# Performance work log

Measured on AMD Instinct MI355X. Metric: run time of the kernel, lower is better.

Reference implementation:

```python
import jax, jax.numpy as jnp
import numpy as np

N, D, B, E, H = 512, 32, 4, 256, 4
SEP = 256
HD = E // H


def setup_inputs() -> dict:
    key = jax.random.key(0)
    ks = jax.random.split(key, 8)
    s = 0.02
    return {
        "src": jax.random.normal(ks[0], (N, D, B, E), dtype=jnp.float32),
        "w_in_row": jax.random.normal(ks[1], (3 * E, E), dtype=jnp.float32) * s,
        "b_in_row": jnp.zeros((3 * E,), jnp.float32),
        "w_out_row": jax.random.normal(ks[2], (E, E), dtype=jnp.float32) * s,
        "b_out_row": jnp.zeros((E,), jnp.float32),
        "w_in_col": jax.random.normal(ks[3], (3 * E, E), dtype=jnp.float32) * s,
        "b_in_col": jnp.zeros((3 * E,), jnp.float32),
        "w_out_col": jax.random.normal(ks[4], (E, E), dtype=jnp.float32) * s,
        "b_out_col": jnp.zeros((E,), jnp.float32),
        "ln_g": jnp.ones((E,), jnp.float32),
        "ln_b": jnp.zeros((E,), jnp.float32),
        "task_ids": jax.random.randint(ks[5], (B,), 0, 10),
        "single_eval_position": SEP,
    }


def _mha(x, w_in, b_in, w_out, b_out, mask):
    # x: (S, Bt, E); torch MultiheadAttention with batch_first=False
    S, Bt, _ = x.shape
    qkv = x @ w_in.T + b_in                      # (S, Bt, 3E)
    q, k, v = jnp.split(qkv, 3, axis=-1)
    to_heads = lambda t: t.reshape(S, Bt, H, HD).transpose(1, 2, 0, 3)  # (Bt,H,S,HD)
    q, k, v = to_heads(q), to_heads(k), to_heads(v)
    scores = jnp.einsum('bhqd,bhkd->bhqk', q, k) * (HD ** -0.5)
    if mask is not None:  # mask True == disallowed (torch convention)
        scores = jnp.where(mask[None, None], -jnp.inf, scores)
    attn = jax.nn.softmax(scores, axis=-1)
    out = jnp.einsum('bhqk,bhkd->bhqd', attn, v)
    out = out.transpose(2, 0, 1, 3).reshape(S, Bt, E)
    return out @ w_out.T + b_out


def _layer_norm(x, g, b, eps=1e-5):
    mu = x.mean(-1, keepdims=True)
    var = ((x - mu) ** 2).mean(-1, keepdims=True)
    return (x - mu) / jnp.sqrt(var + eps) * g + b


def reference(src, w_in_row, b_in_row, w_out_row, b_out_row,
              w_in_col, b_in_col, w_out_col, b_out_col,
              ln_g, ln_b, task_ids, single_eval_position):
    sep = single_eval_position
    idx = jnp.arange(N)
    # block mask: test queries may not attend to test keys
    row_mask = (idx[:, None] >= sep) & (idx[None, :] >= sep)
    # row attention over the N axis, batched across D*B
    src_row = _mha(src.reshape(N, D * B, E), w_in_row, b_in_row,
                   w_out_row, b_out_row, row_mask).reshape(N, D, B, E)
    # column attention over the D axis, batched across N*B (no mask)
    x_col = src.transpose(1, 0, 2, 3).reshape(D, N * B, E)
    src_col = _mha(x_col, w_in_col, b_in_col, w_out_col, b_out_col,
                   None).reshape(D, N, B, E).transpose(1, 0, 2, 3)
    # parallel axial (seq_axial=False), post-norm (pre_norm=False): row_norm unused
    return _layer_norm(src + src_row + src_col, ln_g, ln_b)
```

## Files before the change

kernel.cpp:

```cpp
#include <hip/hip_runtime.h>
#include <hip/hip_bf16.h>
#include <cstdint>
#include <cstddef>


typedef __hip_bfloat16 bf16;
typedef __attribute__((ext_vector_type(8))) short bf16x8;
typedef __attribute__((ext_vector_type(8))) short short8;
typedef __attribute__((ext_vector_type(4))) short bf16x4;
typedef __attribute__((ext_vector_type(4))) float f32x4;

#define NN 512
#define DD 32
#define BB 4
#define EE 256
#define HH 4
#define HDIM 64
#define DB (DD*BB)
#define MTOK (NN*DD*BB)
#define KBLK 64
#define QSCALE 0.1803368801f

extern "C" __device__ float __ocml_exp2_f32(float);

__device__ __forceinline__ float bf2f(bf16 x){ return __bfloat162float(x); }
__device__ __forceinline__ short pkbf(float x){
  union { float f; uint32_t u; } c; c.f = x;
  return (short)((c.u + 0x8000u) >> 16);
}

#define AS1C(p) ((const __attribute__((address_space(1))) void*)(p))
#define AS3(p)  ((__attribute__((address_space(3))) void*)(p))

__global__ __launch_bounds__(256) void cvt_main(
    const float* __restrict__ src, const float* __restrict__ wirf,
    const float* __restrict__ wicf, bf16* __restrict__ src_bf,
    bf16* __restrict__ wir, bf16* __restrict__ wic)
{
  const int b = blockIdx.x;
  const float* s; bf16* d; int off;
  if (b < 8192)      { s = src;  d = src_bf; off = b; }
  else if (b < 8288) { s = wirf; d = wir;    off = b - 8192; }
  else               { s = wicf; d = wic;    off = b - 8288; }
  const int i = (off * 256 + threadIdx.x) * 8;
  const float* p = s + i;
  short8 o;
  #pragma unroll
  for (int j = 0; j < 8; ++j) ((short*)&o)[j] = pkbf(p[j]);
  *(short8*)(d + i) = o;
}

__global__ __launch_bounds__(256) void cvt_w2_kernel(
    const float* __restrict__ orr, const float* __restrict__ oc,
    bf16* __restrict__ d_or, bf16* __restrict__ d_oc)
{
  const int b = blockIdx.x;
  const float* src = (b < 32) ? orr : oc;
  bf16* dst = (b < 32) ? d_or : d_oc;
  const int off = (b < 32) ? b : b - 32;
  const int i = (off * 256 + threadIdx.x) * 8;
  const float* p = src + i;
  short8 o;
  #pragma unroll
  for (int j = 0; j < 8; ++j) ((short*)&o)[j] = pkbf(p[j]);
  *(short8*)(dst + i) = o;
}

template<int NT>
__global__ __launch_bounds__(256,2) void gemm_qkv(
    const bf16* __restrict__ A, const bf16* __restrict__ W1,
    const bf16* __restrict__ W2, const float* __restrict__ b1,
    const float* __restrict__ b2, bf16* __restrict__ C,
    const int nt1, const int nout)
{
  __shared__ bf16 As[128][64];
  __shared__ bf16 Bs[128][64];
  const int bid = blockIdx.x;
  const int xcd = bid & 7;
  const int i0  = bid >> 3;
  const int bm  = xcd * 64 + i0 / NT;
  const int bn  = i0 % NT;
  const int lbn = (bn < nt1) ? bn : bn - nt1;
  const bf16* W = (bn < nt1) ? W1 : W2;
  const float* bias = (bn < nt1) ? b1 : b2;

  const int tid  = threadIdx.x;
  const int wid  = tid >> 6;
  const int lane = tid & 63;
  const int lo = lane & 15, hi = lane >> 4;
  const int wr = wid >> 1, wc = wid & 1;

  const int srow = lane >> 3;
  const int ssrc = ((lane & 7) << 4) ^ (srow << 4);

  f32x4 acc[4][4] = {};

  for (int k0 = 0; k0 < 256; k0 += 64) {
    __syncthreads();
    #pragma unroll
    for (int i = 0; i < 4; ++i) {
      const int r = wid * 32 + i * 8 + srow;
      const int m = bm * 128 + r;
      const char* gpA = (const char*)(A + (size_t)m * EE + k0) + ssrc;
      __builtin_amdgcn_global_load_lds(AS1C(gpA), AS3(&As[wid*32 + i*8][0]), 16, 0, 0);
      const int wn = lbn * 128 + r;
      const char* gpB = (const char*)(W + (size_t)wn * EE + k0) + ssrc;
      __builtin_amdgcn_global_load_lds(AS1C(gpB), AS3(&Bs[wid*32 + i*8][0]), 16, 0, 0);
    }
    __syncthreads();

    #pragma unroll
    for (int kc = 0; kc < 2; ++kc) {
      const int cc = kc * 64 + hi * 16;
      bf16x8 af[4], bfr[4];
      #pragma unroll
      for (int i = 0; i < 4; ++i) {
        const int ra = wr * 64 + i * 16 + lo;
        af[i]  = *(const bf16x8*)((const char*)&As[ra][0] + (cc ^ ((ra & 7) << 4)));
        const int rb = wc * 64 + i * 16 + lo;
        bfr[i] = *(const bf16x8*)((const char*)&Bs[rb][0] + (cc ^ ((rb & 7) << 4)));
      }
      __builtin_amdgcn_s_setprio(1);
      #pragma unroll
      for (int mi = 0; mi < 4; ++mi)
        #pragma unroll
        for (int ni = 0; ni < 4; ++ni)
          acc[mi][ni] = __builtin_amdgcn_mfma_f32_16x16x32_bf16(
              af[mi], bfr[ni], acc[mi][ni], 0, 0, 0);
      __builtin_amdgcn_s_setprio(0);
    }
  }

  float bv[4];
  #pragma unroll
  for (int ni = 0; ni < 4; ++ni)
    bv[ni] = bias[lbn * 128 + wc * 64 + ni * 16 + lo];

  #pragma unroll
  for (int mi = 0; mi < 4; ++mi) {
    #pragma unroll
    for (int r = 0; r < 4; ++r) {
      const int m = bm * 128 + wr * 64 + mi * 16 + hi * 4 + r;
      #pragma unroll
      for (int ni = 0; ni < 4; ++ni) {
        const int col = bn * 128 + wc * 64 + ni * 16 + lo;
        C[(size_t)m * nout + col] = __hip_bfloat16_raw{(unsigned short)pkbf(acc[mi][ni][r] + bv[ni])};
      }
    }
  }
}

__global__ __launch_bounds__(256,2) void gemm_oproj(
    const bf16* __restrict__ A1, const bf16* __restrict__ A2,
    const bf16* __restrict__ W1, const bf16* __restrict__ W2,
    const float* __restrict__ b1, const float* __restrict__ b2,
    bf16* __restrict__ C)
{
  __shared__ bf16 As[128][64];
  __shared__ bf16 Bs[128][64];
  const int bid = blockIdx.x;
  const int xcd = bid & 7;
  const int i0  = bid >> 3;
  const int bm  = xcd * 64 + (i0 >> 1);
  const int bn  = i0 & 1;

  const int tid  = threadIdx.x;
  const int wid  = tid >> 6;
  const int lane = tid & 63;
  const int lo = lane & 15, hi = lane >> 4;
  const int wr = wid >> 1, wc = wid & 1;

  const int srow = lane >> 3;
  const int ssrc = ((lane & 7) << 4) ^ (srow << 4);

  f32x4 acc[4][4] = {};

  for (int k0 = 0; k0 < 512; k0 += 64) {
    const bf16* A = (k0 < 256) ? A1 : A2;
    const bf16* W = (k0 < 256) ? W1 : W2;
    const int kk = k0 & 255;
    __syncthreads();
    #pragma unroll
    for (int i = 0; i < 4; ++i) {
      const int r = wid * 32 + i * 8 + srow;
      const int m = bm * 128 + r;
      const char* gpA = (const char*)(A + (size_t)m * EE + kk) + ssrc;
      __builtin_amdgcn_global_load_lds(AS1C(gpA), AS3(&As[wid*32 + i*8][0]), 16, 0, 0);
      const int wn = bn * 128 + r;
      const char* gpB = (const char*)(W + (size_t)wn * EE + kk) + ssrc;
      __builtin_amdgcn_global_load_lds(AS1C(gpB), AS3(&Bs[wid*32 + i*8][0]), 16, 0, 0);
    }
    __syncthreads();

    #pragma unroll
    for (int kc = 0; kc < 2; ++kc) {
      const int cc = kc * 64 + hi * 16;
      bf16x8 af[4], bfr[4];
      #pragma unroll
      for (int i = 0; i < 4; ++i) {
        const int ra = wr * 64 + i * 16 + lo;
        af[i]  = *(const bf16x8*)((const char*)&As[ra][0] + (cc ^ ((ra & 7) << 4)));
        const int rb = wc * 64 + i * 16 + lo;
        bfr[i] = *(const bf16x8*)((const char*)&Bs[rb][0] + (cc ^ ((rb & 7) << 4)));
      }
      __builtin_amdgcn_s_setprio(1);
      #pragma unroll
      for (int mi = 0; mi < 4; ++mi)
        #pragma unroll
        for (int ni = 0; ni < 4; ++ni)
          acc[mi][ni] = __builtin_amdgcn_mfma_f32_16x16x32_bf16(
              af[mi], bfr[ni], acc[mi][ni], 0, 0, 0);
      __builtin_amdgcn_s_setprio(0);
    }
  }

  float bv[4];
  #pragma unroll
  for (int ni = 0; ni < 4; ++ni) {
    const int col = bn * 128 + wc * 64 + ni * 16 + lo;
    bv[ni] = b1[col] + b2[col];
  }

  #pragma unroll
  for (int mi = 0; mi < 4; ++mi) {
    #pragma unroll
    for (int r = 0; r < 4; ++r) {
      const int m = bm * 128 + wr * 64 + mi * 16 + hi * 4 + r;
      #pragma unroll
      for (int ni = 0; ni < 4; ++ni) {
        const int col = bn * 128 + wc * 64 + ni * 16 + lo;
        C[(size_t)m * EE + col] = __hip_bfloat16_raw{(unsigned short)pkbf(acc[mi][ni][r] + bv[ni])};
      }
    }
  }
}

__global__ __launch_bounds__(256,4) void attn_axial(
    const bf16* __restrict__ baseR, const bf16* __restrict__ baseC,
    const int stride, bf16* __restrict__ attnR, bf16* __restrict__ attnC,
    const int* __restrict__ sep_ptr, const int nrow)
{
  __shared__ bf16 smem[9216];
  const int tid  = threadIdx.x;
  const int lane = tid & 63;
  const int lo = lane & 15, hi = lane >> 4;

  if ((int)blockIdx.x < nrow) {
    const int bid = blockIdx.x;
    const int xcd = bid & 7;
    const int idx = bid >> 3;
    const int pair = xcd * 64 + (idx >> 3);
    const int qt = idx & 7;
    const int t = pair >> 2;
    const int h = pair & 3;
    const int sep = *sep_ptr;
    const int wid = tid >> 6;
    bf16* Ks = smem;
    bf16* Vt = smem + 4608;

    const int qb = qt * 64;
    const int q0 = qb + wid * 16;

    bf16x8 qf[2];
    {
      const bf16* Qp = baseR + ((size_t)(q0 + lo) * DB + t) * stride + h * HDIM;
      bf16x8 a = *(const bf16x8*)(Qp + hi * 8);
      bf16x8 b = *(const bf16x8*)(Qp + 32 + hi * 8);
      #pragma unroll
      for (int j = 0; j < 8; ++j) {
        ((short*)&qf[0])[j] = pkbf(bf2f(((const bf16*)&a)[j]) * QSCALE);
        ((short*)&qf[1])[j] = pkbf(bf2f(((const bf16*)&b)[j]) * QSCALE);
      }
    }

    const int kr  = tid >> 2;
    const int kc4 = (tid & 3) * 16;
    const int vr  = tid & 63;
    const int vc  = (tid >> 6) * 16;
    const bf16* Kbase = baseR + ((size_t)kr * DB + t) * stride + EE + h * HDIM + kc4;
    const bf16* Vbase = baseR + ((size_t)vr * DB + t) * stride + 2*EE + h * HDIM + vc;
    const size_t kstep = (size_t)KBLK * DB * stride;

    f32x4 Oa[4] = {};
    float m_run = -1e30f, l_run = 0.f;

    const int nkt = (qb >= sep) ? ((sep + KBLK - 1) >> 6) : (NN >> 6);
    const bool need_mask = (qb + 64 > sep) && (nkt * KBLK > sep);

    bf16x8 kg0 = *(const bf16x8*)(Kbase);
    bf16x8 kg1 = *(const bf16x8*)(Kbase + 8);
    bf16x8 vg0 = *(const bf16x8*)(Vbase);
    bf16x8 vg1 = *(const bf16x8*)(Vbase + 8);

    for (int kt = 0; kt < nkt; ++kt) {
      const int k0 = kt * KBLK;

      *(bf16x8*)&Ks[kr*72 + kc4]     = kg0;
      *(bf16x8*)&Ks[kr*72 + kc4 + 8] = kg1;
      #pragma unroll
      for (int j = 0; j < 8; ++j) {
        Vt[(vc + j)*72 + vr]     = ((const bf16*)&vg0)[j];
        Vt[(vc + 8 + j)*72 + vr] = ((const bf16*)&vg1)[j];
      }
      __syncthreads();

      if (kt + 1 < nkt) {
        const size_t off = (size_t)(kt + 1) * kstep;
        kg0 = *(const bf16x8*)(Kbase + off);
        kg1 = *(const bf16x8*)(Kbase + off + 8);
        vg0 = *(const bf16x8*)(Vbase + off);
        vg1 = *(const bf16x8*)(Vbase + off + 8);
      }

      f32x4 st[4];
      {
        bf16x8 kf[4][2];
        #pragma unroll
        for (int kb = 0; kb < 4; ++kb)
          #pragma unroll
          for (int kc = 0; kc < 2; ++kc)
            kf[kb][kc] = *(const bf16x8*)&Ks[(kb*16 + lo)*72 + kc*32 + hi*8];
        __builtin_amdgcn_s_setprio(1);
        #pragma unroll
        for (int kb = 0; kb < 4; ++kb) {
          st[kb] = (f32x4){0,0,0,0};
          #pragma unroll
          for (int kc = 0; kc < 2; ++kc)
            st[kb] = __builtin_amdgcn_mfma_f32_16x16x32_bf16(
                kf[kb][kc], qf[kc], st[kb], 0, 0, 0);
        }
        __builtin_amdgcn_s_setprio(0);
      }

      if (need_mask && k0 + KBLK > sep) {
        const int qq = q0 + lo;
        #pragma unroll
        for (int kb = 0; kb < 4; ++kb)
          #pragma unroll
          for (int r = 0; r < 4; ++r) {
            const int kk = k0 + kb*16 + 4*hi + r;
            if (qq >= sep && kk >= sep) st[kb][r] = -1e30f;
          }
      }

      float mx = -1e30f;
      #pragma unroll
      for (int kb = 0; kb < 4; ++kb)
        #pragma unroll
        for (int r = 0; r < 4; ++r) mx = fmaxf(mx, st[kb][r]);
      mx = fmaxf(mx, __shfl_xor(mx, 16));
      mx = fmaxf(mx, __shfl_xor(mx, 32));

      if (__any(mx - m_run > 5.f)) {
        const float mn = fmaxf(m_run, mx);
        const float corr = __ocml_exp2_f32(m_run - mn);
        m_run = mn;
        l_run *= corr;
        float c4[4];
        #pragma unroll
        for (int r = 0; r < 4; ++r) c4[r] = __shfl(corr, hi*4 + r);
        #pragma unroll
        for (int n = 0; n < 4; ++n)
          #pragma unroll
          for (int r = 0; r < 4; ++r) Oa[n][r] *= c4[r];
      }

      float s0 = 0.f;
      #pragma unroll
      for (int kb = 0; kb < 4; ++kb)
        #pragma unroll
        for (int r = 0; r < 4; ++r) {
          const float pv = __ocml_exp2_f32(st[kb][r] - m_run);
          st[kb][r] = pv;
          s0 += pv;
        }
      s0 += __shfl_xor(s0, 16);
      s0 += __shfl_xor(s0, 32);
      l_run += s0;

      bf16x8 pa[2];
      #pragma unroll
      for (int kc = 0; kc < 2; ++kc)
        #pragma unroll
        for (int j = 0; j < 8; ++j)
          ((short*)&pa[kc])[j] = pkbf(st[kc*2 + (j>>2)][j&3]);

      __builtin_amdgcn_s_setprio(1);
      #pragma unroll
      for (int n = 0; n < 4; ++n) {
        #pragma unroll
        for (int kc = 0; kc < 2; ++kc) {
          const bf16* vrow = &Vt[(n*16 + lo)*72];
          bf16x4 v0 = *(const bf16x4*)(vrow + kc*32 + 4*hi);
          bf16x4 v1 = *(const bf16x4*)(vrow + kc*32 + 16 + 4*hi);
          bf16x8 vf = __builtin_shufflevector(v0, v1, 0,1,2,3,4,5,6,7);
          Oa[n] = __builtin_amdgcn_mfma_f32_16x16x32_bf16(pa[kc], vf, Oa[n], 0, 0, 0);
        }
      }
      __builtin_amdgcn_s_setprio(0);
      __syncthreads();
    }

    float linv[4];
    #pragma unroll
    for (int r = 0; r < 4; ++r) linv[r] = 1.f / __shfl(l_run, hi*4 + r);
    #pragma unroll
    for (int r = 0; r < 4; ++r) {
      const int qq = q0 + hi*4 + r;
      bf16* Op = attnR + ((size_t)qq * DB + t) * EE + h * HDIM;
      #pragma unroll
      for (int n = 0; n < 4; ++n)
        Op[n*16 + lo] = __hip_bfloat16_raw{(unsigned short)pkbf(Oa[n][r] * linv[r])};
    }
  } else {
    const int cb = blockIdx.x - nrow;
    const int n = cb >> 2;
    const int b = cb & 3;
    const int h = tid >> 6;

    {
      const int k  = tid & 31;
      const int hh = tid >> 6;
      const int dh = ((tid >> 5) & 1) * 32;
      const bf16* Vp = baseC + ((size_t)(n*DB + k*4 + b)) * stride + 2*EE + hh*64 + dh;
      #pragma unroll
      for (int c = 0; c < 4; ++c) {
        bf16x8 vv = *(const bf16x8*)(Vp + c*8);
        #pragma unroll
        for (int j = 0; j < 8; ++j)
          smem[hh*2304 + (dh + c*8 + j)*36 + k] = ((const bf16*)&vv)[j];
      }
    }

    bf16x8 qf[2][2], kf[2][2];
    #pragma unroll
    for (int mt = 0; mt < 2; ++mt) {
      const bf16* Qp = baseC + ((size_t)(n*DB + (mt*16 + lo)*4 + b)) * stride + h*64;
      #pragma unroll
      for (int kc = 0; kc < 2; ++kc) {
        bf16x8 v = *(const bf16x8*)(Qp + kc*32 + hi*8);
        #pragma unroll
        for (int j = 0; j < 8; ++j)
          ((short*)&v)[j] = pkbf(bf2f(((const bf16*)&v)[j]) * QSCALE);
        qf[mt][kc] = v;
      }
      const bf16* Kp = Qp + EE;
      kf[mt][0] = *(const bf16x8*)(Kp + hi*8);
      kf[mt][1] = *(const bf16x8*)(Kp + 32 + hi*8);
    }
    __syncthreads();

    f32x4 st[2][2];
    #pragma unroll
    for (int kt = 0; kt < 2; ++kt)
      #pragma unroll
      for (int mt = 0; mt < 2; ++mt) {
        f32x4 a = {0,0,0,0};
        a = __builtin_amdgcn_mfma_f32_16x16x32_bf16(kf[kt][0], qf[mt][0], a, 0, 0, 0);
        a = __builtin_amdgcn_mfma_f32_16x16x32_bf16(kf[kt][1], qf[mt][1], a, 0, 0, 0);
        st[kt][mt] = a;
      }

    float l[2];
    #pragma unroll
    for (int mt = 0; mt < 2; ++mt) {
      float mx = -1e30f;
      #pragma unroll
      for (int kt = 0; kt < 2; ++kt)
        #pragma unroll
        for (int r = 0; r < 4; ++r) mx = fmaxf(mx, st[kt][mt][r]);
      mx = fmaxf(mx, __shfl_xor(mx, 16));
      mx = fmaxf(mx, __shfl_xor(mx, 32));
      float s0 = 0.f;
      #pragma unroll
      for (int kt = 0; kt < 2; ++kt)
        #pragma unroll
        for (int r = 0; r < 4; ++r) {
          const float pv = __ocml_exp2_f32(st[kt][mt][r] - mx);
          st[kt][mt][r] = pv;
          s0 += pv;
        }
      s0 += __shfl_xor(s0, 16);
      s0 += __shfl_xor(s0, 32);
      l[mt] = s0;
    }

    bf16x8 pa[2];
    #pragma unroll
    for (int mt = 0; mt < 2; ++mt)
      #pragma unroll
      for (int j = 0; j < 8; ++j)
        ((short*)&pa[mt])[j] = pkbf(st[j>>2][mt][j&3]);

    f32x4 Oa[2][4] = {};
    #pragma unroll
    for (int nn = 0; nn < 4; ++nn) {
      const bf16* vrow = &smem[h*2304 + (nn*16 + lo)*36];
      bf16x4 v0 = *(const bf16x4*)(vrow + 4*hi);
      bf16x4 v1 = *(const bf16x4*)(vrow + 16 + 4*hi);
      bf16x8 vf = __builtin_shufflevector(v0, v1, 0,1,2,3,4,5,6,7);
      Oa[0][nn] = __builtin_amdgcn_mfma_f32_16x16x32_bf16(pa[0], vf, Oa[0][nn], 0, 0, 0);
      Oa[1][nn] = __builtin_amdgcn_mfma_f32_16x16x32_bf16(pa[1], vf, Oa[1][nn], 0, 0, 0);
    }

    float linv[2][4];
    #pragma unroll
    for (int mt = 0; mt < 2; ++mt)
      #pragma unroll
      for (int r = 0; r < 4; ++r)
        linv[mt][r] = 1.f / __shfl(l[mt], hi*4 + r);
    #pragma unroll
    for (int mt = 0; mt < 2; ++mt) {
      #pragma unroll
      for (int r = 0; r < 4; ++r) {
        const int q = mt*16 + hi*4 + r;
        bf16* Op = attnC + ((size_t)(n*DB + q*4 + b)) * EE + h*64;
        #pragma unroll
        for (int nn = 0; nn < 4; ++nn)
          Op[nn*16 + lo] = __hip_bfloat16_raw{(unsigned short)pkbf(Oa[mt][nn][r] * linv[mt][r])};
      }
    }
  }
}

__global__ __launch_bounds__(256) void ln_kernel(
    const float* __restrict__ src, const bf16* __restrict__ rc,
    const float* __restrict__ g, const float* __restrict__ b,
    float* __restrict__ out)
{
  const int m = blockIdx.x * 4 + (threadIdx.x >> 6);
  const int lane = threadIdx.x & 63;
  const float4 s4 = ((const float4*)src)[(size_t)m*64 + lane];
  const bf16x4 r4 = ((const bf16x4*)rc)[(size_t)m*64 + lane];
  float x[4];
  x[0] = s4.x + bf2f(((const bf16*)&r4)[0]);
  x[1] = s4.y + bf2f(((const bf16*)&r4)[1]);
  x[2] = s4.z + bf2f(((const bf16*)&r4)[2]);
  x[3] = s4.w + bf2f(((const bf16*)&r4)[3]);
  float sum = x[0] + x[1] + x[2] + x[3];
  #pragma unroll
  for (int off = 1; off < 64; off <<= 1) sum += __shfl_xor(sum, off);
  const float mu = sum * (1.f/EE);
  float d[4];
  #pragma unroll
  for (int j = 0; j < 4; ++j) d[j] = x[j] - mu;
  float ss = d[0]*d[0] + d[1]*d[1] + d[2]*d[2] + d[3]*d[3];
  #pragma unroll
  for (int off = 1; off < 64; off <<= 1) ss += __shfl_xor(ss, off);
  const float rstd = rsqrtf(ss * (1.f/EE) + 1e-5f);
  const float4 g4 = ((const float4*)g)[lane];
  const float4 b4 = ((const float4*)b)[lane];
  float4 o;
  o.x = d[0] * rstd * g4.x + b4.x;
  o.y = d[1] * rstd * g4.y + b4.y;
  o.z = d[2] * rstd * g4.z + b4.z;
  o.w = d[3] * rstd * g4.w + b4.w;
  ((float4*)out)[(size_t)m*64 + lane] = o;
}

extern "C" void kernel_launch(void* const* d_in, const int* in_sizes, int n_in,
                              void* d_out, int out_size, void* d_ws, size_t ws_size,
                              hipStream_t stream)
{
  const float* src      = (const float*)d_in[0];
  const float* w_in_row = (const float*)d_in[1];
  const float* b_in_row = (const float*)d_in[2];
  const float* w_out_row= (const float*)d_in[3];
  const float* b_out_row= (const float*)d_in[4];
  const float* w_in_col = (const float*)d_in[5];
  const float* b_in_col = (const float*)d_in[6];
  const float* w_out_col= (const float*)d_in[7];
  const float* b_out_col= (const float*)d_in[8];
  const float* ln_g     = (const float*)d_in[9];
  const float* ln_b     = (const float*)d_in[10];
  const int*   sep_ptr  = (const int*)d_in[12];
  float* out = (float*)d_out;

  char* ws = (char*)d_ws;
  dim3 blk(256);

  if (ws_size >= 268435456ULL) {
    bf16* qkv    = (bf16*)(ws);
    bf16* attnR  = (bf16*)(ws + 201326592);
    bf16* attnC  = (bf16*)(ws + 234881024);
    bf16* src_bf = attnR;
    bf16* wir    = (bf16*)(ws + 234881024);
    bf16* wic    = (bf16*)(ws + 235274240);
    bf16* wor    = (bf16*)(ws + 67108864);
    bf16* woc    = (bf16*)(ws + 67239936);
    bf16* rc     = (bf16*)(ws);

    cvt_main<<<dim3(8384), blk, 0, stream>>>(src, w_in_row, w_in_col,
                                             src_bf, wir, wic);
    gemm_qkv<12><<<dim3(512*12), blk, 0, stream>>>(
        src_bf, wir, wic, b_in_row, b_in_col, qkv, 6, 1536);
    attn_axial<<<dim3(6144), blk, 0, stream>>>(
        qkv, qkv + 768, 1536, attnR, attnC, sep_ptr, 4096);
    cvt_w2_kernel<<<dim3(64), blk, 0, stream>>>(w_out_row, w_out_col, wor, woc);
    gemm_oproj<<<dim3(1024), blk, 0, stream>>>(
        attnR, attnC, wor, woc, b_out_row, b_out_col, rc);
    ln_kernel<<<dim3(MTOK/4), blk, 0, stream>>>(src, rc, ln_g, ln_b, out);
  } else {
    bf16* qkv    = (bf16*)(ws);
    bf16* attnR  = (bf16*)(ws + 100663296);
    bf16* attnC  = (bf16*)(ws + 134217728);
    bf16* src_bf = (bf16*)(ws + 167772160);
    bf16* wir    = (bf16*)(ws + 201326592);
    bf16* wic    = (bf16*)(ws + 201719808);
    bf16* wor    = (bf16*)(ws + 67108864);
    bf16* woc    = (bf16*)(ws + 67239936);
    bf16* rc     = (bf16*)(ws);

    cvt_main<<<dim3(8384), blk, 0, stream>>>(src, w_in_row, w_in_col,
                                             src_bf, wir, wic);
    gemm_qkv<6><<<dim3(512*6), blk, 0, stream>>>(
        src_bf, wir, wir, b_in_row, b_in_row, qkv, 6, 768);
    attn_axial<<<dim3(4096), blk, 0, stream>>>(
        qkv, qkv, 768, attnR, attnC, sep_ptr, 4096);
    gemm_qkv<6><<<dim3(512*6), blk, 0, stream>>>(
        src_bf, wic, wic, b_in_col, b_in_col, qkv, 6, 768);
    attn_axial<<<dim3(2048), blk, 0, stream>>>(
        qkv, qkv, 768, attnR, attnC, sep_ptr, 0);
    cvt_w2_kernel<<<dim3(64), blk, 0, stream>>>(w_out_row, w_out_col, wor, woc);
    gemm_oproj<<<dim3(1024), blk, 0, stream>>>(
        attnR, attnC, wor, woc, b_out_row, b_out_col, rc);
    ln_kernel<<<dim3(MTOK/4), blk, 0, stream>>>(src, rc, ln_g, ln_b, out);
  }
}
```

Before: 245.1 us.

## Process two 16-row query fragments per wave in row attention

Each wave in the row-attention path now handles 32 queries as two MFMA fragments, so a block covers 128 queries and half as many row blocks are launched. Each K/V tile staged in shared memory is reused for twice as many queries, which halves global K/V loads and LDS staging per query. The cost is more registers per wave (two sets of accumulators and softmax state), which may lower occupancy, and fewer blocks in the grid.

```diff
diff --git a/kernel.cpp b/kernel.cpp
--- a/kernel.cpp
+++ b/kernel.cpp
@@ -249,8 +249,8 @@
     const int bid = blockIdx.x;
     const int xcd = bid & 7;
     const int idx = bid >> 3;
-    const int pair = xcd * 64 + (idx >> 3);
-    const int qt = idx & 7;
+    const int pair = xcd * 64 + (idx >> 2);
+    const int qt = idx & 3;
     const int t = pair >> 2;
     const int h = pair & 3;
     const int sep = *sep_ptr;
@@ -258,18 +258,19 @@
     bf16* Ks = smem;
     bf16* Vt = smem + 4608;
 
-    const int qb = qt * 64;
-    const int q0 = qb + wid * 16;
-
-    bf16x8 qf[2];
-    {
-      const bf16* Qp = baseR + ((size_t)(q0 + lo) * DB + t) * stride + h * HDIM;
+    const int qb = qt * 128;
+    const int q0 = qb + wid * 32;
+
+    bf16x8 qf[2][2];
+    #pragma unroll
+    for (int mf = 0; mf < 2; ++mf) {
+      const bf16* Qp = baseR + ((size_t)(q0 + mf*16 + lo) * DB + t) * stride + h * HDIM;
       bf16x8 a = *(const bf16x8*)(Qp + hi * 8);
       bf16x8 b = *(const bf16x8*)(Qp + 32 + hi * 8);
       #pragma unroll
       for (int j = 0; j < 8; ++j) {
-        ((short*)&qf[0])[j] = pkbf(bf2f(((const bf16*)&a)[j]) * QSCALE);
-        ((short*)&qf[1])[j] = pkbf(bf2f(((const bf16*)&b)[j]) * QSCALE);
+        ((short*)&qf[mf][0])[j] = pkbf(bf2f(((const bf16*)&a)[j]) * QSCALE);
+        ((short*)&qf[mf][1])[j] = pkbf(bf2f(((const bf16*)&b)[j]) * QSCALE);
       }
     }
 
@@ -281,11 +282,12 @@
     const bf16* Vbase = baseR + ((size_t)vr * DB + t) * stride + 2*EE + h * HDIM + vc;
     const size_t kstep = (size_t)KBLK * DB * stride;
 
-    f32x4 Oa[4] = {};
-    float m_run = -1e30f, l_run = 0.f;
+    f32x4 Oa[2][4] = {};
+    float m_run[2] = {-1e30f, -1e30f};
+    float l_run[2] = {0.f, 0.f};
 
     const int nkt = (qb >= sep) ? ((sep + KBLK - 1) >> 6) : (NN >> 6);
-    const bool need_mask = (qb + 64 > sep) && (nkt * KBLK > sep);
+    const bool need_mask = (qb + 128 > sep) && (nkt * KBLK > sep);
 
     bf16x8 kg0 = *(const bf16x8*)(Kbase);
     bf16x8 kg1 = *(const bf16x8*)(Kbase + 8);
@@ -312,78 +314,77 @@
         vg1 = *(const bf16x8*)(Vbase + off + 8);
       }
 
-      f32x4 st[4];
-      {
-        bf16x8 kf[4][2];
+      f32x4 st[2][4];
+      #pragma unroll
+      for (int kb = 0; kb < 4; ++kb) {
+        bf16x8 kf0 = *(const bf16x8*)&Ks[(kb*16 + lo)*72 + hi*8];
+        bf16x8 kf1 = *(const bf16x8*)&Ks[(kb*16 + lo)*72 + 32 + hi*8];
+        __builtin_amdgcn_s_setprio(1);
+        st[0][kb] = __builtin_amdgcn_mfma_f32_16x16x32_bf16(kf0, qf[0][0], (f32x4){0,0,0,0}, 0, 0, 0);
+        st[0][kb] = __builtin_amdgcn_mfma_f32_16x16x32_bf16(kf1, qf[0][1], st[0][kb], 0, 0, 0);
+        st[1][kb] = __builtin_amdgcn_mfma_f32_16x16x32_bf16(kf0, qf[1][0], (f32x4){0,0,0,0}, 0, 0, 0);
+        st[1][kb] = __builtin_amdgcn_mfma_f32_16x16x32_bf16(kf1, qf[1][1], st[1][kb], 0, 0, 0);
+        __builtin_amdgcn_s_setprio(0);
+      }
+
+      if (need_mask && k0 + KBLK > sep) {
+        #pragma unroll
+        for (int mf = 0; mf < 2; ++mf) {
+          const int qq = q0 + mf*16 + lo;
+          #pragma unroll
+          for (int kb = 0; kb < 4; ++kb)
+            #pragma unroll
+            for (int r = 0; r < 4; ++r) {
+              const int kk = k0 + kb*16 + 4*hi + r;
+              if (qq >= sep && kk >= sep) st[mf][kb][r] = -1e30f;
+            }
+        }
+      }
+
+      bf16x8 pa[2][2];
+      #pragma unroll
+      for (int mf = 0; mf < 2; ++mf) {
+        float mx = -1e30f;
         #pragma unroll
         for (int kb = 0; kb < 4; ++kb)
           #pragma unroll
-          for (int kc = 0; kc < 2; ++kc)
-            kf[kb][kc] = *(const bf16x8*)&Ks[(kb*16 + lo)*72 + kc*32 + hi*8];
-        __builtin_amdgcn_s_setprio(1);
-        #pragma unroll
-        for (int kb = 0; kb < 4; ++kb) {
-          st[kb] = (f32x4){0,0,0,0};
+          for (int r = 0; r < 4; ++r) mx = fmaxf(mx, st[mf][kb][r]);
+        mx = fmaxf(mx, __shfl_xor(mx, 16));
+        mx = fmaxf(mx, __shfl_xor(mx, 32));
+
+        if (__any(mx - m_run[mf] > 5.f)) {
+          const float mn = fmaxf(m_run[mf], mx);
+          const float corr = __ocml_exp2_f32(m_run[mf] - mn);
+          m_run[mf] = mn;
+          l_run[mf] *= corr;
+          float c4[4];
           #pragma unroll
-          for (int kc = 0; kc < 2; ++kc)
-            st[kb] = __builtin_amdgcn_mfma_f32_16x16x32_bf16(
-                kf[kb][kc], qf[kc], st[kb], 0, 0, 0);
+          for (int r = 0; r < 4; ++r) c4[r] = __shfl(corr, hi*4 + r);
+          #pragma unroll
+          for (int n = 0; n < 4; ++n)
+            #pragma unroll
+            for (int r = 0; r < 4; ++r) Oa[mf][n][r] *= c4[r];
         }
-        __builtin_amdgcn_s_setprio(0);
-      }
-
-      if (need_mask && k0 + KBLK > sep) {
-        const int qq = q0 + lo;
+
+        float s0 = 0.f;
         #pragma unroll
         for (int kb = 0; kb < 4; ++kb)
           #pragma unroll
           for (int r = 0; r < 4; ++r) {
-            const int kk = k0 + kb*16 + 4*hi + r;
-            if (qq >= sep && kk >= sep) st[kb][r] = -1e30f;
+            const float pv = __ocml_exp2_f32(st[mf][kb][r] - m_run[mf]);
+            st[mf][kb][r] = pv;
+            s0 += pv;
           }
-      }
-
-      float mx = -1e30f;
-      #pragma unroll
-      for (int kb = 0; kb < 4; ++kb)
-        #pragma unroll
-        for (int r = 0; r < 4; ++r) mx = fmaxf(mx, st[kb][r]);
-      mx = fmaxf(mx, __shfl_xor(mx, 16));
-      mx = fmaxf(mx, __shfl_xor(mx, 32));
-
-      if (__any(mx - m_run > 5.f)) {
-        const float mn = fmaxf(m_run, mx);
-        const float corr = __ocml_exp2_f32(m_run - mn);
-        m_run = mn;
-        l_run *= corr;
-        float c4[4];
-        #pragma unroll
-        for (int r = 0; r < 4; ++r) c4[r] = __shfl(corr, hi*4 + r);
-        #pragma unroll
-        for (int n = 0; n < 4; ++n)
+        s0 += __shfl_xor(s0, 16);
+        s0 += __shfl_xor(s0, 32);
+        l_run[mf] += s0;
+
+        #pragma unroll
+        for (int kc = 0; kc < 2; ++kc)
           #pragma unroll
-          for (int r = 0; r < 4; ++r) Oa[n][r] *= c4[r];
-      }
-
-      float s0 = 0.f;
-      #pragma unroll
-      for (int kb = 0; kb < 4; ++kb)
-        #pragma unroll
-        for (int r = 0; r < 4; ++r) {
-          const float pv = __ocml_exp2_f32(st[kb][r] - m_run);
-          st[kb][r] = pv;
-          s0 += pv;
-        }
-      s0 += __shfl_xor(s0, 16);
-      s0 += __shfl_xor(s0, 32);
-      l_run += s0;
-
-      bf16x8 pa[2];
-      #pragma unroll
-      for (int kc = 0; kc < 2; ++kc)
-        #pragma unroll
-        for (int j = 0; j < 8; ++j)
-          ((short*)&pa[kc])[j] = pkbf(st[kc*2 + (j>>2)][j&3]);
+          for (int j = 0; j < 8; ++j)
+            ((short*)&pa[mf][kc])[j] = pkbf(st[mf][kc*2 + (j>>2)][j&3]);
+      }
 
       __builtin_amdgcn_s_setprio(1);
       #pragma unroll
@@ -394,23 +395,27 @@
           bf16x4 v0 = *(const bf16x4*)(vrow + kc*32 + 4*hi);
           bf16x4 v1 = *(const bf16x4*)(vrow + kc*32 + 16 + 4*hi);
           bf16x8 vf = __builtin_shufflevector(v0, v1, 0,1,2,3,4,5,6,7);
-          Oa[n] = __builtin_amdgcn_mfma_f32_16x16x32_bf16(pa[kc], vf, Oa[n], 0, 0, 0);
+          Oa[0][n] = __builtin_amdgcn_mfma_f32_16x16x32_bf16(pa[0][kc], vf, Oa[0][n], 0, 0, 0);
+          Oa[1][n] = __builtin_amdgcn_mfma_f32_16x16x32_bf16(pa[1][kc], vf, Oa[1][n], 0, 0, 0);
         }
       }
       __builtin_amdgcn_s_setprio(0);
       __syncthreads();
     }
 
-    float linv[4];
-    #pragma unroll
-    for (int r = 0; r < 4; ++r) linv[r] = 1.f / __shfl(l_run, hi*4 + r);
-    #pragma unroll
-    for (int r = 0; r < 4; ++r) {
-      const int qq = q0 + hi*4 + r;
-      bf16* Op = attnR + ((size_t)qq * DB + t) * EE + h * HDIM;
-      #pragma unroll
-      for (int n = 0; n < 4; ++n)
-        Op[n*16 + lo] = __hip_bfloat16_raw{(unsigned short)pkbf(Oa[n][r] * linv[r])};
+    #pragma unroll
+    for (int mf = 0; mf < 2; ++mf) {
+      float linv[4];
+      #pragma unroll
+      for (int r = 0; r < 4; ++r) linv[r] = 1.f / __shfl(l_run[mf], hi*4 + r);
+      #pragma unroll
+      for (int r = 0; r < 4; ++r) {
+        const int qq = q0 + mf*16 + hi*4 + r;
+        bf16* Op = attnR + ((size_t)qq * DB + t) * EE + h * HDIM;
+        #pragma unroll
+        for (int n = 0; n < 4; ++n)
+          Op[n*16 + lo] = __hip_bfloat16_raw{(unsigned short)pkbf(Oa[mf][n][r] * linv[r])};
+      }
     }
   } else {
     const int cb = blockIdx.x - nrow;
@@ -594,8 +599,8 @@
                                              src_bf, wir, wic);
     gemm_qkv<12><<<dim3(512*12), blk, 0, stream>>>(
         src_bf, wir, wic, b_in_row, b_in_col, qkv, 6, 1536);
-    attn_axial<<<dim3(6144), blk, 0, stream>>>(
-        qkv, qkv + 768, 1536, attnR, attnC, sep_ptr, 4096);
+    attn_axial<<<dim3(4096), blk, 0, stream>>>(
+        qkv, qkv + 768, 1536, attnR, attnC, sep_ptr, 2048);
     cvt_w2_kernel<<<dim3(64), blk, 0, stream>>>(w_out_row, w_out_col, wor, woc);
     gemm_oproj<<<dim3(1024), blk, 0, stream>>>(
         attnR, attnC, wor, woc, b_out_row, b_out_col, rc);
@@ -615,8 +620,8 @@
                                              src_bf, wir, wic);
     gemm_qkv<6><<<dim3(512*6), blk, 0, stream>>>(
         src_bf, wir, wir, b_in_row, b_in_row, qkv, 6, 768);
-    attn_axial<<<dim3(4096), blk, 0, stream>>>(
-        qkv, qkv, 768, attnR, attnC, sep_ptr, 4096);
+    attn_axial<<<dim3(2048), blk, 0, stream>>>(
+        qkv, qkv, 768, attnR, attnC, sep_ptr, 2048);
     gemm_qkv<6><<<dim3(512*6), blk, 0, stream>>>(
         src_bf, wic, wic, b_in_col, b_in_col, qkv, 6, 768);
     attn_axial<<<dim3(2048), blk, 0, stream>>>(
```

Result: slower. 258.2 us (+5.3%).
